# Kernel tuning notes

Hardware: AMD Instinct MI355X
Metric: run time of the kernel (lower is better)

Reference implementation:

```python
import jax, jax.numpy as jnp
import numpy as np

S, P = 64, 32          # scenes, pedestrians per scene (uniform)
N = S * P              # total pedestrians = 2048
H, E = 64, 64          # h_dim, embedding_dim
D1, D2 = 512, 1024     # mlp_pre_pool hidden, bottleneck_dim
EPS = 1e-5             # torch BatchNorm1d eps


def _batchnorm(x, gamma, beta):
    # Training-mode BN with per-scene batch stats (matches the per-scene
    # loop in the original, where BN sees one scene's num_ped^2 rows).
    # x: [S, P*P, D]
    mu = jnp.mean(x, axis=1, keepdims=True)
    var = jnp.mean(jnp.square(x - mu), axis=1, keepdims=True)  # biased var, as torch BN
    return (x - mu) * jax.lax.rsqrt(var + EPS) * gamma + beta


def setup_inputs() -> dict:
    key = jax.random.key(0)
    ks = jax.random.split(key, 16)
    h_states = jax.random.normal(ks[0], (1, N, H), jnp.float32)
    starts = jnp.arange(S, dtype=jnp.int32) * P
    seq_start_end = jnp.stack([starts, starts + P], axis=1)  # [S, 2]
    end_pos = jax.random.normal(ks[1], (N, 2), jnp.float32)
    rel_pos = jax.random.normal(ks[2], (N, 2), jnp.float32)  # unused (pooling_dim=2) but a fwd arg
    sc = 0.05
    params = dict(
        W_embed=jax.random.normal(ks[3], (2, E), jnp.float32) * sc,
        b_embed=jnp.zeros((E,), jnp.float32),
        W1=jax.random.normal(ks[4], (E + H, D1), jnp.float32) * sc,
        b1=jnp.zeros((D1,), jnp.float32),
        g1=jnp.ones((D1,), jnp.float32),
        be1=jnp.zeros((D1,), jnp.float32),
        W2=jax.random.normal(ks[5], (D1, D2), jnp.float32) * sc,
        b2=jnp.zeros((D2,), jnp.float32),
        g2=jnp.ones((D2,), jnp.float32),
        be2=jnp.zeros((D2,), jnp.float32),
    )
    return dict(h_states=h_states, seq_start_end=seq_start_end,
                end_pos=end_pos, rel_pos=rel_pos, **params)


def reference(h_states, seq_start_end, end_pos, rel_pos,
              W_embed, b_embed, W1, b1, g1, be1, W2, b2, g2, be2):
    # Uniform scenes: seq_start_end delimits S contiguous blocks of P peds.
    pos = end_pos.reshape(S, P, 2)
    h = h_states.reshape(N, H).reshape(S, P, H)
    # Original indexing: row (k*P + j) -> pos[j] - pos[k], hidden[j];
    # the final view(P, P, -1).max(1) maxes over j for each k.
    rel = pos[:, None, :, :] - pos[:, :, None, :]          # [S, Pk, Pj, 2]
    emb = rel @ W_embed + b_embed                          # [S, Pk, Pj, E]
    hid = jnp.broadcast_to(h[:, None, :, :], (S, P, P, H)) # hidden of j
    x = jnp.concatenate([emb, hid], axis=-1).reshape(S, P * P, E + H)
    x = jax.nn.relu(_batchnorm(x @ W1 + b1, g1, be1))      # [S, P*P, 512]
    x = jax.nn.relu(_batchnorm(x @ W2 + b2, g2, be2))      # [S, P*P, 1024]
    pool_h = x.reshape(S, P, P, D2).max(axis=2)            # max over j
    return pool_h.reshape(N, D2)
```

## Files before the change

### kernel.cpp

```cpp
#include <hip/hip_runtime.h>
#include <hip/hip_bf16.h>

#define S_ 64
#define P_ 32
#define N_ 2048
#define H_ 64
#define E_ 64
#define D1_ 512
#define D2_ 1024
#define EPS_ 1e-5f

typedef unsigned short u16;
using bf16x8 = __attribute__((ext_vector_type(8))) __bf16;
using floatx4 = __attribute__((ext_vector_type(4))) float;

__device__ inline u16 f2bf(float x) {
    unsigned u = __float_as_uint(x);
    unsigned r = (u + 0x7fffu + ((u >> 16) & 1u)) >> 16;
    return (u16)r;
}


__device__ void prep_scene_256(int u, int tid, float* smem,
                               const float* __restrict__ pos, const float* __restrict__ h,
                               const float* __restrict__ We, const float* __restrict__ W1,
                               const float* __restrict__ g1, const float* __restrict__ be1,
                               float* __restrict__ A, float* __restrict__ Bv) {
    const int s = u >> 2, dq = u & 3;
    const int jg = tid >> 7, dl = tid & 127;
    const int d = (dq << 7) + dl;
    float* hs = smem;
    float* ps = smem + 2048;
    float* red = smem + 2112;
    for (int i = tid; i < 2048; i += 256) hs[i] = h[(size_t)s * 2048 + i];
    if (tid < 64) ps[tid] = pos[s * 64 + tid];
    __syncthreads();
    float wq0 = 0.f, wq1 = 0.f;
    for (int e = 0; e < 64; ++e) {
        const float wv = W1[e * 512 + d];
        wq0 += We[e] * wv;
        wq1 += We[64 + e] * wv;
    }
    float w[16], uu[16];
#pragma unroll
    for (int jj = 0; jj < 16; ++jj) w[jj] = 0.f;
    const float4* h4 = (const float4*)hs;
    for (int e4 = 0; e4 < 16; ++e4) {
        const float c0 = W1[(64 + e4 * 4 + 0) * 512 + d];
        const float c1 = W1[(64 + e4 * 4 + 1) * 512 + d];
        const float c2 = W1[(64 + e4 * 4 + 2) * 512 + d];
        const float c3 = W1[(64 + e4 * 4 + 3) * 512 + d];
#pragma unroll
        for (int jj = 0; jj < 16; ++jj) {
            const float4 hv = h4[((jg << 4) + jj) * 16 + e4];
            w[jj] += hv.x * c0 + hv.y * c1 + hv.z * c2 + hv.w * c3;
        }
    }
    float sw = 0.f, sww = 0.f, su = 0.f, suu = 0.f;
#pragma unroll
    for (int jj = 0; jj < 16; ++jj) {
        const int j = (jg << 4) + jj;
        uu[jj] = ps[2 * j] * wq0 + ps[2 * j + 1] * wq1;
        w[jj] += uu[jj];
        sw += w[jj]; sww += w[jj] * w[jj];
        su += uu[jj]; suu += uu[jj] * uu[jj];
    }
    red[(jg << 7) + dl] = sw;
    red[256 + (jg << 7) + dl] = sww;
    red[512 + (jg << 7) + dl] = su;
    red[768 + (jg << 7) + dl] = suu;
    __syncthreads();
    const float tw = red[dl] + red[128 + dl];
    const float tww = red[256 + dl] + red[384 + dl];
    const float tu = red[512 + dl] + red[640 + dl];
    const float tuu = red[768 + dl] + red[896 + dl];
    const float mw = tw * (1.f / 32.f), mu2 = tu * (1.f / 32.f);
    const float var = (tww * (1.f / 32.f) - mw * mw) + (tuu * (1.f / 32.f) - mu2 * mu2);
    const float sc = rsqrtf(var + EPS_) * g1[d];
    const float bb = be1[d];
#pragma unroll
    for (int jj = 0; jj < 16; ++jj) {
        const int j = (jg << 4) + jj;
        A[(size_t)(s * 32 + j) * 512 + d] = (w[jj] - mw) * sc + bb;
        Bv[(size_t)(s * 32 + j) * 512 + d] = (uu[jj] - mu2) * sc;
    }
}

__device__ void w2t_tile_256(int b2, int tid, void* smem,
                             const float* __restrict__ W2, u16* __restrict__ w2t) {
    float (*tile)[65] = (float (*)[65])smem;
    const int bi = b2 & 15, bj = b2 >> 4;
    const int tx = tid & 63, ty = tid >> 6;
#pragma unroll
    for (int i = 0; i < 64; i += 4)
        tile[ty + i][tx] = W2[(size_t)(bj * 64 + ty + i) * 1024 + bi * 64 + tx];
    __syncthreads();
#pragma unroll
    for (int i = 0; i < 64; i += 4)
        w2t[(size_t)(bi * 64 + ty + i) * 512 + bj * 64 + tx] = f2bf(tile[tx][ty + i]);
}

__global__ __launch_bounds__(256, 2)
void k_gemm(const float* __restrict__ A, const float* __restrict__ Bv,
            const u16* __restrict__ w2t,
            float* __restrict__ maxv, float* __restrict__ minv,
            float* __restrict__ psum, float* __restrict__ psumsq) {
    __shared__ __align__(16) u16 As[128 * 64];
    __shared__ __align__(16) u16 Ws[256 * 64];
    const int tid = threadIdx.x;
    const int wave = tid >> 6, lane = tid & 63;
    const int wm = wave >> 1, wn = wave & 1;
    const int quad = lane >> 4, l16 = lane & 15;
    const int lrow = lane >> 3, lchk = lane & 7;
    const int gchk = lchk ^ lrow;
    const int sj = tid >> 3, sc8 = tid & 7;
    const int bid = blockIdx.x;
    const int mt = bid >> 2, cs = bid & 3;
    const int s2 = mt >> 3, rb = mt & 7;
    const int pedb = rb << 2;
    const int N0 = cs << 8;
    const float* Aj = A + ((size_t)(s2 * 32 + sj) << 9) + (sc8 << 3);
    const float* Bp = Bv + ((size_t)(s2 * 32 + pedb) << 9) + (sc8 << 3);
    const int swz = (sc8 ^ (sj & 7)) << 3;

    floatx4 acc[4][8] = {};
    for (int it = 0; it < 8; ++it) {
        const int k0 = it << 6;
#pragma unroll
        for (int t = 0; t < 8; ++t) {
            const int rbase = (wave << 6) + (t << 3);
            const u16* gb = w2t + (size_t)(N0 + rbase + lrow) * 512 + (k0 + (gchk << 3));
            __builtin_amdgcn_global_load_lds(
                (const __attribute__((address_space(1))) void*)gb,
                (__attribute__((address_space(3))) void*)(Ws + (rbase << 6)), 16, 0, 0);
        }
        {
            const float4 alo = *(const float4*)(Aj + k0);
            const float4 ahi = *(const float4*)(Aj + k0 + 4);
#pragma unroll
            for (int p = 0; p < 4; ++p) {
                const int r = (p << 5) + sj;
                const float4 blo = *(const float4*)(Bp + ((size_t)p << 9) + k0);
                const float4 bhi = *(const float4*)(Bp + ((size_t)p << 9) + k0 + 4);
                bf16x8 o;
                o[0] = (__bf16)fmaxf(alo.x - blo.x, 0.f);
                o[1] = (__bf16)fmaxf(alo.y - blo.y, 0.f);
                o[2] = (__bf16)fmaxf(alo.z - blo.z, 0.f);
                o[3] = (__bf16)fmaxf(alo.w - blo.w, 0.f);
                o[4] = (__bf16)fmaxf(ahi.x - bhi.x, 0.f);
                o[5] = (__bf16)fmaxf(ahi.y - bhi.y, 0.f);
                o[6] = (__bf16)fmaxf(ahi.z - bhi.z, 0.f);
                o[7] = (__bf16)fmaxf(ahi.w - bhi.w, 0.f);
                *(bf16x8*)(As + (r << 6) + swz) = o;
            }
        }
        __syncthreads();
#pragma unroll
        for (int kk = 0; kk < 2; ++kk) {
            const int ck = (kk << 2) + quad;
            const int po = (ck ^ (l16 & 7)) << 3;
            bf16x8 af[4], wf[8];
#pragma unroll
            for (int tm = 0; tm < 4; ++tm) {
                const int row = (wm << 6) + (tm << 4) + l16;
                af[tm] = *(const bf16x8*)(As + (row << 6) + po);
            }
#pragma unroll
            for (int tn = 0; tn < 8; ++tn) {
                const int wrow = (wn << 7) + (tn << 4) + l16;
                wf[tn] = *(const bf16x8*)(Ws + (wrow << 6) + ((ck ^ (wrow & 7)) << 3));
            }
#pragma unroll
            for (int tm = 0; tm < 4; ++tm)
#pragma unroll
                for (int tn = 0; tn < 8; ++tn)
                    acc[tm][tn] = __builtin_amdgcn_mfma_f32_16x16x32_bf16(
                        af[tm], wf[tn], acc[tm][tn], 0, 0, 0);
        }
        __syncthreads();
    }
#pragma unroll
    for (int tn = 0; tn < 8; ++tn) {
        const int col = N0 + (wn << 7) + (tn << 4) + l16;
        float wsum = 0.f, wsq = 0.f;
#pragma unroll
        for (int gp = 0; gp < 2; ++gp) {
            float vmax = -3.4e38f, vmin = 3.4e38f, vs = 0.f, vq = 0.f;
#pragma unroll
            for (int tm = gp * 2; tm < gp * 2 + 2; ++tm)
#pragma unroll
                for (int r = 0; r < 4; ++r) {
                    const float v = acc[tm][tn][r];
                    vmax = fmaxf(vmax, v);
                    vmin = fminf(vmin, v);
                    vs += v;
                    vq += v * v;
                }
#pragma unroll
            for (int off = 16; off < 64; off <<= 1) {
                vmax = fmaxf(vmax, __shfl_xor(vmax, off));
                vmin = fminf(vmin, __shfl_xor(vmin, off));
                vs += __shfl_xor(vs, off);
                vq += __shfl_xor(vq, off);
            }
            if (quad == 0) {
                const int kg = s2 * 32 + pedb + (wm << 1) + gp;
                maxv[(size_t)kg * 1024 + col] = vmax;
                minv[(size_t)kg * 1024 + col] = vmin;
            }
            wsum += vs;
            wsq += vq;
        }
        if (quad == 0) {
            const int slot = (s2 << 4) + (rb << 1) + wm;
            psum[(size_t)slot * 1024 + col] = wsum;
            psumsq[(size_t)slot * 1024 + col] = wsq;
        }
    }
}

__global__ __launch_bounds__(256)
void k_prep(const float* __restrict__ pos, const float* __restrict__ h,
            const float* __restrict__ We, const float* __restrict__ W1,
            const float* __restrict__ g1, const float* __restrict__ be1,
            const float* __restrict__ W2,
            float* __restrict__ A, float* __restrict__ Bv, u16* __restrict__ w2t) {
    __shared__ __align__(16) char smem_raw[16912];
    const int bid = blockIdx.x;
    if (bid < 256)
        prep_scene_256(bid, threadIdx.x, (float*)smem_raw, pos, h, We, W1, g1, be1, A, Bv);
    else
        w2t_tile_256(bid - 256, threadIdx.x, smem_raw, W2, w2t);
}

__global__ __launch_bounds__(256)
void k_final(const float* __restrict__ maxv, const float* __restrict__ minv,
             const float* __restrict__ psum, const float* __restrict__ psumsq,
             const float* __restrict__ g2, const float* __restrict__ be2,
             float* __restrict__ out) {
    const int u = blockIdx.x, tid = threadIdx.x;
    const int s3 = u >> 2;
    const int c = ((u & 3) << 8) + tid;
    float sm = 0.f, sq = 0.f;
#pragma unroll
    for (int t = 0; t < 16; ++t) {
        sm += psum[(size_t)(s3 * 16 + t) * 1024 + c];
        sq += psumsq[(size_t)(s3 * 16 + t) * 1024 + c];
    }
    const float mu = sm * (1.f / 1024.f);
    const float var = sq * (1.f / 1024.f) - mu * mu;
    const float inv = rsqrtf(var + EPS_);
    const float scale = g2[c] * inv;
    const float bb = be2[c];
    const float* src = (scale >= 0.f) ? maxv : minv;
    for (int k = 0; k < 32; ++k) {
        const float v = src[(size_t)(s3 * 32 + k) * 1024 + c];
        out[(size_t)(s3 * 32 + k) * 1024 + c] = fmaxf((v - mu) * scale + bb, 0.f);
    }
}

extern "C" void kernel_launch(void* const* d_in, const int* in_sizes, int n_in,
                              void* d_out, int out_size, void* d_ws, size_t ws_size,
                              hipStream_t stream) {
    const float* h_states = (const float*)d_in[0];
    const float* end_pos = (const float*)d_in[2];
    const float* W_embed = (const float*)d_in[4];
    const float* W1 = (const float*)d_in[6];
    const float* g1 = (const float*)d_in[8];
    const float* be1 = (const float*)d_in[9];
    const float* W2 = (const float*)d_in[10];
    const float* g2 = (const float*)d_in[12];
    const float* be2 = (const float*)d_in[13];
    float* out = (float*)d_out;

    float* Abuf = (float*)d_ws;
    float* Bbuf = Abuf + 1048576;
    float* maxv = Bbuf + 1048576;
    float* minv = maxv + 2097152;
    float* psum = minv + 2097152;
    float* psumsq = psum + 1048576;
    u16* w2t = (u16*)(psumsq + 1048576);

    k_prep<<<dim3(384), dim3(256), 0, stream>>>(end_pos, h_states, W_embed, W1,
                                                g1, be1, W2, Abuf, Bbuf, w2t);
    k_gemm<<<dim3(2048), dim3(256), 0, stream>>>(Abuf, Bbuf, w2t, maxv, minv,
                                                 psum, psumsq);
    k_final<<<dim3(256), dim3(256), 0, stream>>>(maxv, minv, psum, psumsq, g2, be2, out);
}
```

Baseline: 181.9 us.

## Double-buffer k_gemm LDS and loop over all N chunks per block

The GEMM kernel now gives each block all four 256-column chunks in a single 32-step loop, launching 512 blocks instead of 2048. The A tile (built from the A/B difference with ReLU) is rebuilt for every chunk. Shared memory is double-buffered: the next W2 tile is staged through global_load_lds and the next A tile is built while MFMAs run on the current buffers. Manual waitcnt and barriers replace the two __syncthreads per step. Occupancy drops to one block per CU with 96KB dynamic LDS, and the in-flight loads add register pressure.

```diff
diff --git a/kernel.cpp b/kernel.cpp
--- a/kernel.cpp
+++ b/kernel.cpp
@@ -100,13 +100,19 @@
         w2t[(size_t)(bi * 64 + ty + i) * 512 + bj * 64 + tx] = f2bf(tile[tx][ty + i]);
 }
 
-__global__ __launch_bounds__(256, 2)
+#define LGKM0() asm volatile("s_waitcnt lgkmcnt(0)" ::: "memory")
+#define VMC10() asm volatile("s_waitcnt vmcnt(10)" ::: "memory")
+#define VM0()   asm volatile("s_waitcnt vmcnt(0)" ::: "memory")
+
+__global__ __launch_bounds__(256, 1)
 void k_gemm(const float* __restrict__ A, const float* __restrict__ Bv,
             const u16* __restrict__ w2t,
             float* __restrict__ maxv, float* __restrict__ minv,
             float* __restrict__ psum, float* __restrict__ psumsq) {
-    __shared__ __align__(16) u16 As[128 * 64];
-    __shared__ __align__(16) u16 Ws[256 * 64];
+    extern __shared__ __align__(16) char lds_raw[];
+    u16* AsB = (u16*)lds_raw;
+    u16* WsB = AsB + 16384;
+
     const int tid = threadIdx.x;
     const int wave = tid >> 6, lane = tid & 63;
     const int wm = wave >> 1, wn = wave & 1;
@@ -114,109 +120,166 @@
     const int lrow = lane >> 3, lchk = lane & 7;
     const int gchk = lchk ^ lrow;
     const int sj = tid >> 3, sc8 = tid & 7;
-    const int bid = blockIdx.x;
-    const int mt = bid >> 2, cs = bid & 3;
+    const int mt = blockIdx.x;
     const int s2 = mt >> 3, rb = mt & 7;
     const int pedb = rb << 2;
-    const int N0 = cs << 8;
     const float* Aj = A + ((size_t)(s2 * 32 + sj) << 9) + (sc8 << 3);
     const float* Bp = Bv + ((size_t)(s2 * 32 + pedb) << 9) + (sc8 << 3);
     const int swz = (sc8 ^ (sj & 7)) << 3;
 
+    float4 ra0, ra1, rb0[4], rb1[4];
     floatx4 acc[4][8] = {};
-    for (int it = 0; it < 8; ++it) {
-        const int k0 = it << 6;
-#pragma unroll
-        for (int t = 0; t < 8; ++t) {
-            const int rbase = (wave << 6) + (t << 3);
-            const u16* gb = w2t + (size_t)(N0 + rbase + lrow) * 512 + (k0 + (gchk << 3));
-            __builtin_amdgcn_global_load_lds(
-                (const __attribute__((address_space(1))) void*)gb,
-                (__attribute__((address_space(3))) void*)(Ws + (rbase << 6)), 16, 0, 0);
+
+#define LOADR(KX)                                                              \
+    do {                                                                       \
+        ra0 = *(const float4*)(Aj + (KX));                                     \
+        ra1 = *(const float4*)(Aj + (KX) + 4);                                 \
+        _Pragma("unroll")                                                      \
+        for (int p = 0; p < 4; ++p) {                                          \
+            rb0[p] = *(const float4*)(Bp + ((size_t)p << 9) + (KX));           \
+            rb1[p] = *(const float4*)(Bp + ((size_t)p << 9) + (KX) + 4);       \
+        }                                                                      \
+    } while (0)
+
+#define BUILDA(DST)                                                            \
+    do {                                                                       \
+        _Pragma("unroll")                                                      \
+        for (int p = 0; p < 4; ++p) {                                          \
+            const int r = (p << 5) + sj;                                       \
+            bf16x8 o;                                                          \
+            o[0] = (__bf16)fmaxf(ra0.x - rb0[p].x, 0.f);                       \
+            o[1] = (__bf16)fmaxf(ra0.y - rb0[p].y, 0.f);                       \
+            o[2] = (__bf16)fmaxf(ra0.z - rb0[p].z, 0.f);                       \
+            o[3] = (__bf16)fmaxf(ra0.w - rb0[p].w, 0.f);                       \
+            o[4] = (__bf16)fmaxf(ra1.x - rb1[p].x, 0.f);                       \
+            o[5] = (__bf16)fmaxf(ra1.y - rb1[p].y, 0.f);                       \
+            o[6] = (__bf16)fmaxf(ra1.z - rb1[p].z, 0.f);                       \
+            o[7] = (__bf16)fmaxf(ra1.w - rb1[p].w, 0.f);                       \
+            *(bf16x8*)((DST) + (r << 6) + swz) = o;                            \
+        }                                                                      \
+    } while (0)
+
+#define STAGEW(DST, NN, KN)                                                    \
+    do {                                                                       \
+        _Pragma("unroll")                                                      \
+        for (int t = 0; t < 8; ++t) {                                          \
+            const int rbase = (wave << 6) + (t << 3);                          \
+            const u16* gb = w2t + (size_t)((NN) + rbase + lrow) * 512 +        \
+                            ((KN) + (gchk << 3));                              \
+            __builtin_amdgcn_global_load_lds(                                  \
+                (const __attribute__((address_space(1))) void*)gb,             \
+                (__attribute__((address_space(3))) void*)((DST) + (rbase << 6)), \
+                16, 0, 0);                                                     \
+        }                                                                      \
+    } while (0)
+
+#define MFMAK(ABUF, WBUF, KK)                                                  \
+    do {                                                                       \
+        const int ck = ((KK) << 2) + quad;                                     \
+        const int po = (ck ^ (l16 & 7)) << 3;                                  \
+        bf16x8 af[4], wf[8];                                                   \
+        _Pragma("unroll")                                                      \
+        for (int tm = 0; tm < 4; ++tm) {                                       \
+            const int row = (wm << 6) + (tm << 4) + l16;                       \
+            af[tm] = *(const bf16x8*)((ABUF) + (row << 6) + po);               \
+        }                                                                      \
+        _Pragma("unroll")                                                      \
+        for (int tn = 0; tn < 8; ++tn) {                                       \
+            const int wrow = (wn << 7) + (tn << 4) + l16;                      \
+            wf[tn] = *(const bf16x8*)((WBUF) + (wrow << 6) +                   \
+                                      ((ck ^ (wrow & 7)) << 3));               \
+        }                                                                      \
+        _Pragma("unroll")                                                      \
+        for (int tm = 0; tm < 4; ++tm)                                         \
+            _Pragma("unroll")                                                  \
+            for (int tn = 0; tn < 8; ++tn)                                     \
+                acc[tm][tn] = __builtin_amdgcn_mfma_f32_16x16x32_bf16(         \
+                    af[tm], wf[tn], acc[tm][tn], 0, 0, 0);                     \
+    } while (0)
+
+    LOADR(0);
+    BUILDA(AsB);
+    STAGEW(WsB, 0, 0);
+    LOADR(64);
+    VMC10();
+    LGKM0();
+    __builtin_amdgcn_s_barrier();
+
+#pragma unroll 2
+    for (int u = 0; u < 32; ++u) {
+        const int buf = u & 1;
+        const u16* Ac = AsB + (buf << 13);
+        const u16* Wc = WsB + (buf << 14);
+        u16* An = AsB + ((buf ^ 1) << 13);
+        u16* Wn = WsB + ((buf ^ 1) << 14);
+
+        if (u < 31) STAGEW(Wn, ((u + 1) >> 3) << 8, ((u + 1) & 7) << 6);
+        MFMAK(Ac, Wc, 0);
+        if (u < 31) BUILDA(An);
+        MFMAK(Ac, Wc, 1);
+        if (u < 30) {
+            LOADR(((u + 2) & 7) << 6);
+            VMC10();
+        } else if (u == 30) {
+            VM0();
         }
-        {
-            const float4 alo = *(const float4*)(Aj + k0);
-            const float4 ahi = *(const float4*)(Aj + k0 + 4);
-#pragma unroll
-            for (int p = 0; p < 4; ++p) {
-                const int r = (p << 5) + sj;
-                const float4 blo = *(const float4*)(Bp + ((size_t)p << 9) + k0);
-                const float4 bhi = *(const float4*)(Bp + ((size_t)p << 9) + k0 + 4);
-                bf16x8 o;
-                o[0] = (__bf16)fmaxf(alo.x - blo.x, 0.f);
-                o[1] = (__bf16)fmaxf(alo.y - blo.y, 0.f);
-                o[2] = (__bf16)fmaxf(alo.z - blo.z, 0.f);
-                o[3] = (__bf16)fmaxf(alo.w - blo.w, 0.f);
-                o[4] = (__bf16)fmaxf(ahi.x - bhi.x, 0.f);
-                o[5] = (__bf16)fmaxf(ahi.y - bhi.y, 0.f);
-                o[6] = (__bf16)fmaxf(ahi.z - bhi.z, 0.f);
-                o[7] = (__bf16)fmaxf(ahi.w - bhi.w, 0.f);
-                *(bf16x8*)(As + (r << 6) + swz) = o;
+
+        if ((u & 7) == 7) {
+            const int N0 = (u >> 3) << 8;
+#pragma unroll
+            for (int tn = 0; tn < 8; ++tn) {
+                const int col = N0 + (wn << 7) + (tn << 4) + l16;
+                float wsum = 0.f, wsq = 0.f;
+#pragma unroll
+                for (int gp = 0; gp < 2; ++gp) {
+                    float vmax = -3.4e38f, vmin = 3.4e38f, vs = 0.f, vq = 0.f;
+#pragma unroll
+                    for (int tm = gp * 2; tm < gp * 2 + 2; ++tm)
+#pragma unroll
+                        for (int r = 0; r < 4; ++r) {
+                            const float v = acc[tm][tn][r];
+                            vmax = fmaxf(vmax, v);
+                            vmin = fminf(vmin, v);
+                            vs += v;
+                            vq += v * v;
+                        }
+#pragma unroll
+                    for (int off = 16; off < 64; off <<= 1) {
+                        vmax = fmaxf(vmax, __shfl_xor(vmax, off));
+                        vmin = fminf(vmin, __shfl_xor(vmin, off));
+                        vs += __shfl_xor(vs, off);
+                        vq += __shfl_xor(vq, off);
+                    }
+                    if (quad == 0) {
+                        const int kg = s2 * 32 + pedb + (wm << 1) + gp;
+                        maxv[(size_t)kg * 1024 + col] = vmax;
+                        minv[(size_t)kg * 1024 + col] = vmin;
+                    }
+                    wsum += vs;
+                    wsq += vq;
+                }
+                if (quad == 0) {
+                    const int slot = (s2 << 4) + (rb << 1) + wm;
+                    psum[(size_t)slot * 1024 + col] = wsum;
+                    psumsq[(size_t)slot * 1024 + col] = wsq;
+                }
             }
+#pragma unroll
+            for (int tm = 0; tm < 4; ++tm)
+#pragma unroll
+                for (int tn = 0; tn < 8; ++tn)
+                    acc[tm][tn] = floatx4{0.f, 0.f, 0.f, 0.f};
         }
-        __syncthreads();
-#pragma unroll
-        for (int kk = 0; kk < 2; ++kk) {
-            const int ck = (kk << 2) + quad;
-            const int po = (ck ^ (l16 & 7)) << 3;
-            bf16x8 af[4], wf[8];
-#pragma unroll
-            for (int tm = 0; tm < 4; ++tm) {
-                const int row = (wm << 6) + (tm << 4) + l16;
-                af[tm] = *(const bf16x8*)(As + (row << 6) + po);
-            }
-#pragma unroll
-            for (int tn = 0; tn < 8; ++tn) {
-                const int wrow = (wn << 7) + (tn << 4) + l16;
-                wf[tn] = *(const bf16x8*)(Ws + (wrow << 6) + ((ck ^ (wrow & 7)) << 3));
-            }
-#pragma unroll
-            for (int tm = 0; tm < 4; ++tm)
-#pragma unroll
-                for (int tn = 0; tn < 8; ++tn)
-                    acc[tm][tn] = __builtin_amdgcn_mfma_f32_16x16x32_bf16(
-                        af[tm], wf[tn], acc[tm][tn], 0, 0, 0);
+
+        if (u < 31) {
+            LGKM0();
+            __builtin_amdgcn_s_barrier();
         }
-        __syncthreads();
-    }
-#pragma unroll
-    for (int tn = 0; tn < 8; ++tn) {
-        const int col = N0 + (wn << 7) + (tn << 4) + l16;
-        float wsum = 0.f, wsq = 0.f;
-#pragma unroll
-        for (int gp = 0; gp < 2; ++gp) {
-            float vmax = -3.4e38f, vmin = 3.4e38f, vs = 0.f, vq = 0.f;
-#pragma unroll
-            for (int tm = gp * 2; tm < gp * 2 + 2; ++tm)
-#pragma unroll
-                for (int r = 0; r < 4; ++r) {
-                    const float v = acc[tm][tn][r];
-                    vmax = fmaxf(vmax, v);
-                    vmin = fminf(vmin, v);
-                    vs += v;
-                    vq += v * v;
-                }
-#pragma unroll
-            for (int off = 16; off < 64; off <<= 1) {
-                vmax = fmaxf(vmax, __shfl_xor(vmax, off));
-                vmin = fminf(vmin, __shfl_xor(vmin, off));
-                vs += __shfl_xor(vs, off);
-                vq += __shfl_xor(vq, off);
-            }
-            if (quad == 0) {
-                const int kg = s2 * 32 + pedb + (wm << 1) + gp;
-                maxv[(size_t)kg * 1024 + col] = vmax;
-                minv[(size_t)kg * 1024 + col] = vmin;
-            }
-            wsum += vs;
-            wsq += vq;
-        }
-        if (quad == 0) {
-            const int slot = (s2 << 4) + (rb << 1) + wm;
-            psum[(size_t)slot * 1024 + col] = wsum;
-            psumsq[(size_t)slot * 1024 + col] = wsq;
-        }
-    }
+    }
+#undef LOADR
+#undef BUILDA
+#undef STAGEW
+#undef MFMAK
 }
 
 __global__ __launch_bounds__(256)
@@ -281,9 +344,16 @@
     float* psumsq = psum + 1048576;
     u16* w2t = (u16*)(psumsq + 1048576);
 
+    static int lds_opt_in = 0;
+    if (!lds_opt_in) {
+        hipFuncSetAttribute(reinterpret_cast<const void*>(k_gemm),
+                            hipFuncAttributeMaxDynamicSharedMemorySize, 98304);
+        lds_opt_in = 1;
+    }
+
     k_prep<<<dim3(384), dim3(256), 0, stream>>>(end_pos, h_states, W_embed, W1,
                                                 g1, be1, W2, Abuf, Bbuf, w2t);
-    k_gemm<<<dim3(2048), dim3(256), 0, stream>>>(Abuf, Bbuf, w2t, maxv, minv,
-                                                 psum, psumsq);
+    k_gemm<<<dim3(512), dim3(256), 98304, stream>>>(Abuf, Bbuf, w2t, maxv, minv,
+                                                    psum, psumsq);
     k_final<<<dim3(256), dim3(256), 0, stream>>>(maxv, minv, psum, psumsq, g2, be2, out);
 }
```

New measurement: 226.1 us. 24.3% more time.

## Fuse final BN2+ReLU into GEMM via per-scene last-block counter

Applied to the files above, without the earlier changes.

Removes the separate finalize kernel. Each GEMM block bumps a per-scene atomic counter, and the last of the 32 blocks for a scene reduces the partial sums and writes the normalized, ReLU'd output. The GEMM now stores only the max or min extreme, picked by the sign of g2, instead of both, which halves those writes. MFMA sections also get raised wave priority through s_setprio. This saves one launch and some memory traffic, but the finishing block does serial tail work, and it depends on counters being reset in the prep kernel and on fence ordering.

```diff
diff --git a/kernel.cpp b/kernel.cpp
--- a/kernel.cpp
+++ b/kernel.cpp
@@ -103,10 +103,13 @@
 __global__ __launch_bounds__(256, 2)
 void k_gemm(const float* __restrict__ A, const float* __restrict__ Bv,
             const u16* __restrict__ w2t,
-            float* __restrict__ maxv, float* __restrict__ minv,
-            float* __restrict__ psum, float* __restrict__ psumsq) {
+            const float* __restrict__ g2, const float* __restrict__ be2,
+            float* __restrict__ ext, float* __restrict__ psum,
+            float* __restrict__ psumsq, int* __restrict__ cnt,
+            float* __restrict__ out) {
     __shared__ __align__(16) u16 As[128 * 64];
     __shared__ __align__(16) u16 Ws[256 * 64];
+    __shared__ int lastv;
     const int tid = threadIdx.x;
     const int wave = tid >> 6, lane = tid & 63;
     const int wm = wave >> 1, wn = wave & 1;
@@ -170,18 +173,21 @@
                 const int wrow = (wn << 7) + (tn << 4) + l16;
                 wf[tn] = *(const bf16x8*)(Ws + (wrow << 6) + ((ck ^ (wrow & 7)) << 3));
             }
+            __builtin_amdgcn_s_setprio(1);
 #pragma unroll
             for (int tm = 0; tm < 4; ++tm)
 #pragma unroll
                 for (int tn = 0; tn < 8; ++tn)
                     acc[tm][tn] = __builtin_amdgcn_mfma_f32_16x16x32_bf16(
                         af[tm], wf[tn], acc[tm][tn], 0, 0, 0);
+            __builtin_amdgcn_s_setprio(0);
         }
         __syncthreads();
     }
 #pragma unroll
     for (int tn = 0; tn < 8; ++tn) {
         const int col = N0 + (wn << 7) + (tn << 4) + l16;
+        const float g2v = g2[col];
         float wsum = 0.f, wsq = 0.f;
 #pragma unroll
         for (int gp = 0; gp < 2; ++gp) {
@@ -205,8 +211,7 @@
             }
             if (quad == 0) {
                 const int kg = s2 * 32 + pedb + (wm << 1) + gp;
-                maxv[(size_t)kg * 1024 + col] = vmax;
-                minv[(size_t)kg * 1024 + col] = vmin;
+                ext[(size_t)kg * 1024 + col] = (g2v >= 0.f) ? vmax : vmin;
             }
             wsum += vs;
             wsq += vq;
@@ -215,6 +220,30 @@
             const int slot = (s2 << 4) + (rb << 1) + wm;
             psum[(size_t)slot * 1024 + col] = wsum;
             psumsq[(size_t)slot * 1024 + col] = wsq;
+        }
+    }
+
+    __threadfence();
+    if (tid == 0) lastv = atomicAdd(&cnt[s2], 1);
+    __syncthreads();
+    if (lastv == 31) {
+        __threadfence();
+        for (int c = tid; c < 1024; c += 256) {
+            float sm = 0.f, sq = 0.f;
+#pragma unroll
+            for (int t = 0; t < 16; ++t) {
+                sm += psum[(size_t)(s2 * 16 + t) * 1024 + c];
+                sq += psumsq[(size_t)(s2 * 16 + t) * 1024 + c];
+            }
+            const float mu = sm * (1.f / 1024.f);
+            const float var = sq * (1.f / 1024.f) - mu * mu;
+            const float scale = g2[c] * rsqrtf(var + EPS_);
+            const float bb = be2[c];
+            for (int k = 0; k < 32; ++k) {
+                const float v = ext[(size_t)(s2 * 32 + k) * 1024 + c];
+                out[(size_t)(s2 * 32 + k) * 1024 + c] =
+                    fmaxf((v - mu) * scale + bb, 0.f);
+            }
         }
     }
 }
@@ -224,39 +253,15 @@
             const float* __restrict__ We, const float* __restrict__ W1,
             const float* __restrict__ g1, const float* __restrict__ be1,
             const float* __restrict__ W2,
-            float* __restrict__ A, float* __restrict__ Bv, u16* __restrict__ w2t) {
+            float* __restrict__ A, float* __restrict__ Bv, u16* __restrict__ w2t,
+            int* __restrict__ cnt) {
     __shared__ __align__(16) char smem_raw[16912];
     const int bid = blockIdx.x;
+    if (bid == 0 && threadIdx.x < 64) cnt[threadIdx.x] = 0;
     if (bid < 256)
         prep_scene_256(bid, threadIdx.x, (float*)smem_raw, pos, h, We, W1, g1, be1, A, Bv);
     else
         w2t_tile_256(bid - 256, threadIdx.x, smem_raw, W2, w2t);
-}
-
-__global__ __launch_bounds__(256)
-void k_final(const float* __restrict__ maxv, const float* __restrict__ minv,
-             const float* __restrict__ psum, const float* __restrict__ psumsq,
-             const float* __restrict__ g2, const float* __restrict__ be2,
-             float* __restrict__ out) {
-    const int u = blockIdx.x, tid = threadIdx.x;
-    const int s3 = u >> 2;
-    const int c = ((u & 3) << 8) + tid;
-    float sm = 0.f, sq = 0.f;
-#pragma unroll
-    for (int t = 0; t < 16; ++t) {
-        sm += psum[(size_t)(s3 * 16 + t) * 1024 + c];
-        sq += psumsq[(size_t)(s3 * 16 + t) * 1024 + c];
-    }
-    const float mu = sm * (1.f / 1024.f);
-    const float var = sq * (1.f / 1024.f) - mu * mu;
-    const float inv = rsqrtf(var + EPS_);
-    const float scale = g2[c] * inv;
-    const float bb = be2[c];
-    const float* src = (scale >= 0.f) ? maxv : minv;
-    for (int k = 0; k < 32; ++k) {
-        const float v = src[(size_t)(s3 * 32 + k) * 1024 + c];
-        out[(size_t)(s3 * 32 + k) * 1024 + c] = fmaxf((v - mu) * scale + bb, 0.f);
-    }
 }
 
 extern "C" void kernel_launch(void* const* d_in, const int* in_sizes, int n_in,
@@ -275,15 +280,14 @@
 
     float* Abuf = (float*)d_ws;
     float* Bbuf = Abuf + 1048576;
-    float* maxv = Bbuf + 1048576;
-    float* minv = maxv + 2097152;
-    float* psum = minv + 2097152;
+    float* ext = Bbuf + 1048576;
+    float* psum = ext + 2097152;
     float* psumsq = psum + 1048576;
     u16* w2t = (u16*)(psumsq + 1048576);
+    int* cnt = (int*)(w2t + 524288);
 
     k_prep<<<dim3(384), dim3(256), 0, stream>>>(end_pos, h_states, W_embed, W1,
-                                                g1, be1, W2, Abuf, Bbuf, w2t);
-    k_gemm<<<dim3(2048), dim3(256), 0, stream>>>(Abuf, Bbuf, w2t, maxv, minv,
-                                                 psum, psumsq);
-    k_final<<<dim3(256), dim3(256), 0, stream>>>(maxv, minv, psum, psumsq, g2, be2, out);
-}
+                                                g1, be1, W2, Abuf, Bbuf, w2t, cnt);
+    k_gemm<<<dim3(2048), dim3(256), 0, stream>>>(Abuf, Bbuf, w2t, g2, be2,
+                                                 ext, psum, psumsq, cnt, out);
+}
```

After: 443.2 us. 144% more time.
